# Optimization experiments

Measured on AMD Instinct MI355X. Metric: run time of the kernel, lower is better.

The kernel has to match this reference:

```python
import jax, jax.numpy as jnp
import numpy as np

NUM_EMBEDDINGS = 1024
EMBEDDING_DIM = 256
COMMITMENT_COST = 0.25
DECAY = 0.99
EPSILON = 1e-05


def setup_inputs() -> dict:
    key = jax.random.key(0)
    k1, k2, k3 = jax.random.split(key, 3)
    z = jax.random.normal(k1, (32, EMBEDDING_DIM, 32, 32), dtype=jnp.float32)
    codebook = jax.random.normal(k2, (NUM_EMBEDDINGS, EMBEDDING_DIM), dtype=jnp.float32)
    ema_cluster_size = jnp.zeros((NUM_EMBEDDINGS,), dtype=jnp.float32)
    ema_dw = jax.random.normal(k3, (NUM_EMBEDDINGS, EMBEDDING_DIM), dtype=jnp.float32)
    return {"z": z, "codebook": codebook, "ema_cluster_size": ema_cluster_size, "ema_dw": ema_dw}


def reference(z, codebook, ema_cluster_size, ema_dw):
    K, D = codebook.shape
    # (B,C,H,W) -> (B,H,W,C)
    zp = jnp.transpose(z, (0, 2, 3, 1))
    z_flat = zp.reshape(-1, D)  # [N, D]
    N = z_flat.shape[0]

    # squared L2 distances to each code: [N, K]
    distances = (jnp.sum(z_flat ** 2, axis=1, keepdims=True)
                 + jnp.sum(codebook ** 2, axis=1)
                 - 2.0 * z_flat @ codebook.T)
    idx = jnp.argmin(distances, axis=1)  # [N]

    quantized = codebook[idx].reshape(zp.shape)  # [B,H,W,C]

    # training-mode EMA codebook update (one-hot scatter expressed as segment sums)
    counts = jax.ops.segment_sum(jnp.ones((N,), z_flat.dtype), idx, num_segments=K)  # encodings.sum(0)
    dw = jax.ops.segment_sum(z_flat, idx, num_segments=K)                            # encodings.T @ z_flat
    new_cluster_size = ema_cluster_size * DECAY + (1.0 - DECAY) * counts
    new_ema_dw = ema_dw * DECAY + (1.0 - DECAY) * dw
    n = jnp.sum(new_cluster_size)
    cluster_size = (new_cluster_size + EPSILON) / (n + K * EPSILON) * n
    new_codebook = new_ema_dw / cluster_size[:, None]

    commitment_loss = jnp.mean((zp - jax.lax.stop_gradient(quantized)) ** 2)
    loss = COMMITMENT_COST * commitment_loss

    # straight-through estimator
    quantized_st = zp + jax.lax.stop_gradient(quantized - zp)

    avg_probs = counts / N
    perplexity = jnp.exp(-jnp.sum(avg_probs * jnp.log(avg_probs + 1e-10)))

    quantized_out = jnp.transpose(quantized_st, (0, 3, 1, 2))  # back to (B,C,H,W)
    return (quantized_out, loss, perplexity, new_codebook, new_cluster_size, new_ema_dw)
```

## Files before the change

### kernel.cpp

```cpp
#include <hip/hip_runtime.h>
#include <cfloat>
#include <cstdint>

#define B_BATCH 32
#define D_DIM   256
#define HW      1024
#define N_POS   32768
#define K_CODES 1024
#define DECAY_F   0.99f
#define ONE_M_DECAY 0.01f
#define EPS_F   1e-5f

#define OUT_Q    0
#define OUT_LOSS 8388608
#define OUT_PERP 8388609
#define OUT_CB   8388610
#define OUT_NCS  8650754
#define OUT_EDW  8651778


#define WS_COUNTS  0
#define WS_ZNORM   4096
#define WS_BSUM    4100
#define WS_MEMSET  4104
#define WS_CBNORM  4352
#define WS_OFFS    8448
#define WS_CURSOR  12544
#define WS_IDX     16640
#define WS_SORTED  147712
#define WS_CBHI    278784
#define WS_CBLO    803072
#define WS_PART    1327360
#define WS_SCODE   3424512
#define WS_TOTAL   3555584

typedef short s16x8 __attribute__((ext_vector_type(8)));
typedef float f32x4 __attribute__((ext_vector_type(4)));
typedef unsigned long long u64;

__device__ __forceinline__ ushort f2bf_rne(float x) {
    uint u = __float_as_uint(x);
    uint r = (u + 0x7FFF + ((u >> 16) & 1)) >> 16;
    return (ushort)r;
}
__device__ __forceinline__ float bf2f(ushort h) {
    return __uint_as_float(((uint)h) << 16);
}

__device__ __forceinline__ void gload16(const void* g, void* l) {
    __builtin_amdgcn_global_load_lds(
        (const __attribute__((address_space(1))) unsigned*)(uintptr_t)g,
        (__attribute__((address_space(3))) unsigned*)(uintptr_t)l, 16, 0, 0);
}

__global__ __launch_bounds__(256) void prep_ztrans(const float* __restrict__ z,
                                                   const float* __restrict__ cb,
                                                   ushort* __restrict__ zhi,
                                                   ushort* __restrict__ zlo,
                                                   ushort* __restrict__ cbhi,
                                                   ushort* __restrict__ cblo,
                                                   float* __restrict__ cbnorm,
                                                   float* __restrict__ znorm_acc) {
    __shared__ float Zs[32][68];
    __shared__ float red[256];
    const int tid = threadIdx.x;

    if (blockIdx.x >= 512) {
        int wave = tid >> 6;
        int lane = tid & 63;
        int k = (blockIdx.x - 512) * 4 + wave;
        float4 v = *(const float4*)&cb[(size_t)k * D_DIM + lane * 4];
        ushort4 h, l;
        h.x = f2bf_rne(v.x); l.x = f2bf_rne(v.x - bf2f(h.x));
        h.y = f2bf_rne(v.y); l.y = f2bf_rne(v.y - bf2f(h.y));
        h.z = f2bf_rne(v.z); l.z = f2bf_rne(v.z - bf2f(h.z));
        h.w = f2bf_rne(v.w); l.w = f2bf_rne(v.w - bf2f(h.w));
        *(ushort4*)&cbhi[(size_t)k * D_DIM + lane * 4] = h;
        *(ushort4*)&cblo[(size_t)k * D_DIM + lane * 4] = l;
        float s = v.x * v.x + v.y * v.y + v.z * v.z + v.w * v.w;
        #pragma unroll
        for (int off = 32; off >= 1; off >>= 1) s += __shfl_xor(s, off);
        if (lane == 0) cbnorm[k] = s;
        return;
    }

    const int n0  = blockIdx.x * 64;
    const int b   = n0 >> 10;
    const int hw0 = n0 & 1023;
    const float* zb = z + (size_t)b * (D_DIM * HW) + hw0;

    const int zd  = tid >> 4;
    const int zcg = tid & 15;
    const int n   = tid >> 2;
    const int dq  = tid & 3;
    const int zcol = (((n >> 2) ^ (dq << 1)) << 2) | (n & 3);
    float zsum = 0.f;

    for (int d0 = 0; d0 < D_DIM; d0 += 32) {
        __syncthreads();
        #pragma unroll
        for (int p = 0; p < 2; ++p) {
            int d = zd + p * 16;
            int g = zcg ^ (((d >> 3) & 3) << 1);
            float4 v = *(const float4*)&zb[(size_t)(d0 + d) * HW + zcg * 4];
            *(float4*)&Zs[d][g * 4] = v;
        }
        __syncthreads();
        s16x8 hv, lv;
        #pragma unroll
        for (int j = 0; j < 8; ++j) {
            float f = Zs[dq * 8 + j][zcol];
            zsum += f * f;
            ushort hb = f2bf_rne(f);
            ushort lb = f2bf_rne(f - bf2f(hb));
            hv[j] = (short)hb;
            lv[j] = (short)lb;
        }
        *(s16x8*)&zhi[(size_t)(n0 + n) * D_DIM + d0 + dq * 8] = hv;
        *(s16x8*)&zlo[(size_t)(n0 + n) * D_DIM + d0 + dq * 8] = lv;
    }
    red[tid] = zsum;
    __syncthreads();
    for (int s2 = 128; s2 >= 1; s2 >>= 1) {
        if (tid < s2) red[tid] += red[tid + s2];
        __syncthreads();
    }
    if (tid == 0) atomicAdd(znorm_acc, red[0]);
}

__global__ __launch_bounds__(512, 2) void argmin_gemm(const ushort* __restrict__ cbhi,
                                                      const ushort* __restrict__ cblo,
                                                      const ushort* __restrict__ zhi,
                                                      const ushort* __restrict__ zlo,
                                                      const float* __restrict__ cbnorm,
                                                      u64* __restrict__ partial) {
    __shared__ __align__(16) ushort lds[65536];

    const int tid  = threadIdx.x;
    const int wave = tid >> 6;
    const int lane = tid & 63;
    const int col  = lane & 15;
    const int lg   = lane >> 4;
    const int wr   = wave >> 2;
    const int wc   = wave & 3;
    const int blk  = blockIdx.x;
    const int mt = (blk >> 3) & 3;
    const int pt = (blk & 7) | ((blk >> 5) << 3);

    const int srow = tid >> 2;
    const int G    = tid & 3;
    const int sg   = (G ^ ((srow >> 1) & 3)) * 16;
    const char* pAh = (const char*)cbhi + (size_t)(mt * 256 + srow) * 512 + sg;
    const char* pAl = (const char*)cblo + (size_t)(mt * 256 + srow) * 512 + sg;
    const char* pBh = (const char*)zhi  + (size_t)(pt * 256 + srow) * 512 + sg;
    const char* pBl = (const char*)zlo  + (size_t)(pt * 256 + srow) * 512 + sg;
    char* const ldsw = (char*)lds + wave * 1024;

    auto stage_q = [&](int kt, int bsel, int q) {
        char* d = ldsw + bsel * 65536;
        const int kb = kt * 64;
        if (q == 0)      { gload16(pAh + kb, d);         gload16(pAh + kb + 65536, d + 8192);  }
        else if (q == 1) { gload16(pAl + kb, d + 16384); gload16(pAl + kb + 65536, d + 24576); }
        else if (q == 2) { gload16(pBh + kb, d + 32768); gload16(pBh + kb + 65536, d + 40960); }
        else             { gload16(pBl + kb, d + 49152); gload16(pBl + kb + 65536, d + 57344); }
    };

    const char* ldsc = (const char*)lds;
    const int swz  = (lg ^ ((col >> 1) & 3)) * 16;
    const int aoff = (wr * 128 + col) * 64 + swz;
    const int boff = (wc * 64 + col) * 64 + swz;

    f32x4 acc[8][4];
    #pragma unroll
    for (int mi = 0; mi < 8; ++mi)
        #pragma unroll
        for (int ni = 0; ni < 4; ++ni) acc[mi][ni] = {0.f, 0.f, 0.f, 0.f};

    stage_q(0, 0, 0); stage_q(0, 0, 1); stage_q(0, 0, 2); stage_q(0, 0, 3);

#define MM3A(AH, AL, mi, ni)                                                                   \
    acc[mi][ni] = __builtin_amdgcn_mfma_f32_16x16x32_bf16(AH, bh[ni], acc[mi][ni], 0, 0, 0);   \
    acc[mi][ni] = __builtin_amdgcn_mfma_f32_16x16x32_bf16(AH, bl[ni], acc[mi][ni], 0, 0, 0);   \
    acc[mi][ni] = __builtin_amdgcn_mfma_f32_16x16x32_bf16(AL, bh[ni], acc[mi][ni], 0, 0, 0);
#define ROW3(AH, AL, mi) MM3A(AH, AL, mi, 0) MM3A(AH, AL, mi, 1) MM3A(AH, AL, mi, 2) MM3A(AH, AL, mi, 3)

    #pragma unroll
    for (int t = 0; t < 8; ++t) {
        asm volatile("s_waitcnt vmcnt(0)" ::: "memory");
        __builtin_amdgcn_s_barrier();
        __builtin_amdgcn_sched_barrier(0);

        const char* bp = ldsc + (t & 1) * 65536;
        const int nb = (t + 1) & 1;
        s16x8 bh[4], bl[4];
        s16x8 ah0, al0, ah1, al1;

        bh[0] = *(const s16x8*)(bp + 32768 + boff);
        bl[0] = *(const s16x8*)(bp + 49152 + boff);
        bh[1] = *(const s16x8*)(bp + 32768 + boff + 1024);
        bl[1] = *(const s16x8*)(bp + 49152 + boff + 1024);
        bh[2] = *(const s16x8*)(bp + 32768 + boff + 2048);
        bl[2] = *(const s16x8*)(bp + 49152 + boff + 2048);
        bh[3] = *(const s16x8*)(bp + 32768 + boff + 3072);
        bl[3] = *(const s16x8*)(bp + 49152 + boff + 3072);
        ah0 = *(const s16x8*)(bp + aoff);
        al0 = *(const s16x8*)(bp + 16384 + aoff);
        ah1 = *(const s16x8*)(bp + aoff + 1024);
        al1 = *(const s16x8*)(bp + 16384 + aoff + 1024);
        if (t < 7) stage_q(t + 1, nb, 0);
        __builtin_amdgcn_s_setprio(1);
        ROW3(ah0, al0, 0) ROW3(ah1, al1, 1)
        __builtin_amdgcn_s_setprio(0);

        ah0 = *(const s16x8*)(bp + aoff + 2048);
        al0 = *(const s16x8*)(bp + 16384 + aoff + 2048);
        ah1 = *(const s16x8*)(bp + aoff + 3072);
        al1 = *(const s16x8*)(bp + 16384 + aoff + 3072);
        if (t < 7) stage_q(t + 1, nb, 1);
        __builtin_amdgcn_s_setprio(1);
        ROW3(ah0, al0, 2) ROW3(ah1, al1, 3)
        __builtin_amdgcn_s_setprio(0);

        ah0 = *(const s16x8*)(bp + aoff + 4096);
        al0 = *(const s16x8*)(bp + 16384 + aoff + 4096);
        ah1 = *(const s16x8*)(bp + aoff + 5120);
        al1 = *(const s16x8*)(bp + 16384 + aoff + 5120);
        if (t < 7) stage_q(t + 1, nb, 2);
        __builtin_amdgcn_s_setprio(1);
        ROW3(ah0, al0, 4) ROW3(ah1, al1, 5)
        __builtin_amdgcn_s_setprio(0);

        ah0 = *(const s16x8*)(bp + aoff + 6144);
        al0 = *(const s16x8*)(bp + 16384 + aoff + 6144);
        ah1 = *(const s16x8*)(bp + aoff + 7168);
        al1 = *(const s16x8*)(bp + 16384 + aoff + 7168);
        if (t < 7) stage_q(t + 1, nb, 3);
        __builtin_amdgcn_s_setprio(1);
        ROW3(ah0, al0, 6) ROW3(ah1, al1, 7)
        __builtin_amdgcn_s_setprio(0);
    }
#undef ROW3
#undef MM3A

    const int kbase = mt * 256 + wr * 128;
    u64 best[4] = {~0ull, ~0ull, ~0ull, ~0ull};
    #pragma unroll
    for (int mi = 0; mi < 8; ++mi) {
        float4 cn = *(const float4*)&cbnorm[kbase + mi * 16 + lg * 4];
        const float* cnp = (const float*)&cn;
        #pragma unroll
        for (int ni = 0; ni < 4; ++ni) {
            #pragma unroll
            for (int r = 0; r < 4; ++r) {
                float dist = cnp[r] - 2.f * acc[mi][ni][r];
                uint ub = __float_as_uint(dist);
                ub = ub ^ (uint)(((int)ub >> 31) | 0x80000000);
                u64 key = ((u64)ub << 32) | (uint)(kbase + mi * 16 + lg * 4 + r);
                if (key < best[ni]) best[ni] = key;
            }
        }
    }
    #pragma unroll
    for (int ni = 0; ni < 4; ++ni) {
        u64 o = __shfl_xor(best[ni], 16); if (o < best[ni]) best[ni] = o;
        o = __shfl_xor(best[ni], 32); if (o < best[ni]) best[ni] = o;
    }
    u64* kredp = (u64*)lds;
    if (lane < 16) {
        #pragma unroll
        for (int ni = 0; ni < 4; ++ni)
            kredp[(wc * 64 + ni * 16 + lane) * 2 + wr] = best[ni];
    }
    __syncthreads();
    if (tid < 256) {
        u64 a = kredp[tid * 2 + 0];
        u64 b = kredp[tid * 2 + 1]; if (b < a) a = b;
        partial[(size_t)(pt * 256 + tid) * 4 + mt] = a;
    }
}

__global__ __launch_bounds__(256) void combine_kernel(const u64* __restrict__ partial,
                                                      int* __restrict__ idx,
                                                      float* __restrict__ counts,
                                                      float* __restrict__ bsum_acc) {
    __shared__ int hist[1024];
    __shared__ float red[256];
    const int tid = threadIdx.x;
    for (int j = tid; j < 1024; j += 256) hist[j] = 0;
    __syncthreads();
    int n = blockIdx.x * 256 + tid;
    const u64* p = partial + (size_t)n * 4;
    u64 m = p[0];
    #pragma unroll
    for (int j = 1; j < 4; ++j) { u64 v = p[j]; if (v < m) m = v; }
    int k = (int)(m & 1023u);
    idx[n] = k;
    atomicAdd(&hist[k], 1);
    uint ub = (uint)(m >> 32);
    uint u = (ub & 0x80000000u) ? (ub ^ 0x80000000u) : ~ub;
    red[tid] = __uint_as_float(u);
    __syncthreads();
    for (int s2 = 128; s2 >= 1; s2 >>= 1) {
        if (tid < s2) red[tid] += red[tid + s2];
        __syncthreads();
    }
    if (tid == 0) atomicAdd(bsum_acc, red[0]);
    for (int j = tid; j < 1024; j += 256) {
        int c = hist[j];
        if (c) atomicAdd(&counts[j], (float)c);
    }
}

__global__ __launch_bounds__(1024) void small_kernel(const float* __restrict__ ema_cs,
                                                     const float* __restrict__ counts,
                                                     const float* __restrict__ znorm,
                                                     const float* __restrict__ bsum,
                                                     float* __restrict__ out_ncs,
                                                     float* __restrict__ out_perp,
                                                     float* __restrict__ out_loss,
                                                     float* __restrict__ ntot_ws,
                                                     int* __restrict__ offsets,
                                                     int* __restrict__ cursor) {
    __shared__ float s1[1024];
    __shared__ float s2[1024];
    __shared__ int   s3[1024];
    int k = threadIdx.x;
    float cnt = counts[k];
    float ncs = ema_cs[k] * DECAY_F + ONE_M_DECAY * cnt;
    out_ncs[k] = ncs;
    float p = cnt / (float)N_POS;
    s1[k] = ncs;
    s2[k] = p * logf(p + 1e-10f);
    int c = (int)cnt;
    s3[k] = c;
    __syncthreads();
    for (int off = 1; off < 1024; off <<= 1) {
        int v = (k >= off) ? s3[k - off] : 0;
        __syncthreads();
        s3[k] += v;
        __syncthreads();
    }
    int excl = s3[k] - c;
    offsets[k] = excl;
    cursor[k] = excl;
    for (int st = 512; st >= 1; st >>= 1) {
        if (k < st) { s1[k] += s1[k + st]; s2[k] += s2[k + st]; }
        __syncthreads();
    }
    if (k == 0) {
        ntot_ws[0] = s1[0];
        out_perp[0] = expf(-s2[0]);
        out_loss[0] = 0.25f * (znorm[0] + bsum[0]) / 8388608.0f;
    }
}

__global__ __launch_bounds__(256) void scatter_kernel(const int* __restrict__ idx,
                                                      int* __restrict__ cursor,
                                                      int* __restrict__ sorted,
                                                      int* __restrict__ scode,
                                                      float* __restrict__ dw_zero) {
    __shared__ int hist[1024];
    __shared__ int base_s[1024];
    const int tid = threadIdx.x;
    {
        float4 z4 = {0.f, 0.f, 0.f, 0.f};
        size_t e = ((size_t)blockIdx.x * 256 + tid) * 8;
        *(float4*)&dw_zero[e] = z4;
        *(float4*)&dw_zero[e + 4] = z4;
    }
    for (int j = tid; j < 1024; j += 256) hist[j] = 0;
    __syncthreads();
    int n = blockIdx.x * 256 + tid;
    int k = idx[n];
    atomicAdd(&hist[k], 1);
    __syncthreads();
    for (int j = tid; j < 1024; j += 256) {
        int c = hist[j];
        if (c) base_s[j] = atomicAdd(&cursor[j], c);
        hist[j] = 0;
    }
    __syncthreads();
    int rank = atomicAdd(&hist[k], 1);
    int pos = base_s[k] + rank;
    sorted[pos] = n;
    scode[pos] = k;
}

#define DW_CHUNK 64
__global__ __launch_bounds__(256) void dw_chunk_kernel(const ushort* __restrict__ zhi,
                                                       const ushort* __restrict__ zlo,
                                                       const int* __restrict__ sorted,
                                                       const int* __restrict__ scode,
                                                       const int* __restrict__ offsets,
                                                       const float* __restrict__ counts,
                                                       float* __restrict__ dw) {
    __shared__ int sid[DW_CHUNK];
    __shared__ int sk[DW_CHUNK];
    const int tid = threadIdx.x;
    const int p0 = blockIdx.x * DW_CHUNK;
    if (tid < DW_CHUNK) {
        sid[tid] = sorted[p0 + tid];
        sk[tid]  = scode[p0 + tid];
    }
    __syncthreads();
    float acc = 0.f;
    int runstart = 0;
    #pragma unroll 4
    for (int i = 0; i < DW_CHUNK; ++i) {
        int id = sid[i];
        float zv = bf2f(zhi[(size_t)id * D_DIM + tid]) + bf2f(zlo[(size_t)id * D_DIM + tid]);
        acc += zv;
        bool end = (i == DW_CHUNK - 1) || (sk[i + 1] != sk[i]);
        if (end) {
            int k = sk[i];
            int off = offsets[k];
            int cnt = (int)counts[k];
            if (p0 + runstart == off && p0 + i == off + cnt - 1)
                dw[(size_t)k * D_DIM + tid] = acc;
            else
                atomicAdd(&dw[(size_t)k * D_DIM + tid], acc);
            acc = 0.f;
            runstart = i + 1;
        }
    }
}

__global__ __launch_bounds__(256) void tail_fused(const float* __restrict__ cb,
                                                  const int* __restrict__ idx,
                                                  float* __restrict__ outq,
                                                  const float* __restrict__ ema_dw,
                                                  const float* __restrict__ out_ncs,
                                                  const float* __restrict__ ntot_ws,
                                                  float* __restrict__ out_edw,
                                                  float* __restrict__ out_cb) {
    const int tid = threadIdx.x;
    if (blockIdx.x >= 512) {
        int k = blockIdx.x - 512;
        int d = tid;
        float ncs = out_ncs[k];
        float nt = ntot_ws[0];
        float csz = (ncs + EPS_F) / (nt + (float)K_CODES * EPS_F) * nt;
        size_t e = (size_t)k * D_DIM + d;
        float ed = ema_dw[e] * DECAY_F + ONE_M_DECAY * out_edw[e];
        out_edw[e] = ed;
        out_cb[e] = ed / csz;
        return;
    }

    __shared__ float Qs[32][65];
    __shared__ int kidx[64];
    const int n0  = blockIdx.x * 64;
    const int b   = n0 >> 10;
    const int hw0 = n0 & 1023;
    float* ob = outq + (size_t)b * (D_DIM * HW) + hw0;

    if (tid < 64) kidx[tid] = idx[n0 + tid];

    for (int d0 = 0; d0 < D_DIM; d0 += 32) {
        __syncthreads();
        #pragma unroll
        for (int h = 0; h < 2; ++h) {
            int s  = tid + 256 * h;
            int n  = s >> 3;
            int dq = s & 7;
            int k  = kidx[n];
            float4 q = *(const float4*)&cb[(size_t)k * D_DIM + d0 + dq * 4];
            Qs[dq * 4 + 0][n] = q.x;
            Qs[dq * 4 + 1][n] = q.y;
            Qs[dq * 4 + 2][n] = q.z;
            Qs[dq * 4 + 3][n] = q.w;
        }
        __syncthreads();
        #pragma unroll
        for (int j = 0; j < 8; ++j) {
            int v = tid + 256 * j;
            int d = v >> 6;
            int n = v & 63;
            ob[(size_t)(d0 + d) * HW + n] = Qs[d][n];
        }
    }
}

extern "C" void kernel_launch(void* const* d_in, const int* in_sizes, int n_in,
                              void* d_out, int out_size, void* d_ws, size_t ws_size,
                              hipStream_t stream) {
    const float* z       = (const float*)d_in[0];
    const float* cb      = (const float*)d_in[1];
    const float* ema_cs  = (const float*)d_in[2];
    const float* ema_dw  = (const float*)d_in[3];
    float* out = (float*)d_out;

    char* ws = (char*)d_ws;
    float* ws_counts = (float*)(ws + WS_COUNTS);
    float* ws_znorm  = (float*)(ws + WS_ZNORM);
    float* ws_bsum   = (float*)(ws + WS_BSUM);
    float* ws_cbnorm = (float*)(ws + WS_CBNORM);
    int*   ws_offs   = (int*)(ws + WS_OFFS);
    int*   ws_cursor = (int*)(ws + WS_CURSOR);
    int*   ws_idx    = (int*)(ws + WS_IDX);
    int*   ws_sorted = (int*)(ws + WS_SORTED);
    ushort* ws_cbhi  = (ushort*)(ws + WS_CBHI);
    ushort* ws_cblo  = (ushort*)(ws + WS_CBLO);
    u64*   ws_part   = (u64*)(ws + WS_PART);
    int*   ws_scode  = (int*)(ws + WS_SCODE);

    ushort* zhi = (ushort*)out;
    ushort* zlo = zhi + 8388608;

    hipMemsetAsync(d_ws, 0, WS_MEMSET, stream);

    prep_ztrans<<<768, 256, 0, stream>>>(z, cb, zhi, zlo, ws_cbhi, ws_cblo,
                                         ws_cbnorm, ws_znorm);
    argmin_gemm<<<512, 512, 0, stream>>>(ws_cbhi, ws_cblo, zhi, zlo, ws_cbnorm, ws_part);
    combine_kernel<<<N_POS / 256, 256, 0, stream>>>(ws_part, ws_idx, ws_counts, ws_bsum);
    small_kernel<<<1, 1024, 0, stream>>>(ema_cs, ws_counts, ws_znorm, ws_bsum,
                                         out + OUT_NCS, out + OUT_PERP, out + OUT_LOSS,
                                         (float*)(ws + WS_ZNORM) + 1024, ws_offs, ws_cursor);
    scatter_kernel<<<N_POS / 256, 256, 0, stream>>>(ws_idx, ws_cursor, ws_sorted,
                                                    ws_scode, out + OUT_EDW);
    dw_chunk_kernel<<<N_POS / DW_CHUNK, 256, 0, stream>>>(zhi, zlo, ws_sorted, ws_scode,
                                                          ws_offs, ws_counts, out + OUT_EDW);
    tail_fused<<<1536, 256, 0, stream>>>(cb, ws_idx, out + OUT_Q, ema_dw, out + OUT_NCS,
                                         (float*)(ws + WS_ZNORM) + 1024,
                                         out + OUT_EDW, out + OUT_CB);
}
```

Before: 196.8 us.

## Shrink argmin GEMM tile to 256x128 with triple-buffered LDS prefetch

The argmin GEMM block changes from 512 threads with a 256x256 tile to 256 threads with a 256-code by 128-position tile, doubling the grid to 1024 blocks. Staging moves from quartered loads into a double buffer to a three-stage LDS ring that prefetches two k-steps ahead and waits with a partial vmcnt instead of draining all loads. The aim is to hide global load latency better and raise block count. In exchange each codebook tile is reloaded twice as often relative to z, and one block per CU with a larger LDS footprint may lower occupancy.

```diff
diff --git a/kernel.cpp b/kernel.cpp
--- a/kernel.cpp
+++ b/kernel.cpp
@@ -128,21 +128,21 @@
     if (tid == 0) atomicAdd(znorm_acc, red[0]);
 }
 
-__global__ __launch_bounds__(512, 2) void argmin_gemm(const ushort* __restrict__ cbhi,
+__global__ __launch_bounds__(256, 1) void argmin_gemm(const ushort* __restrict__ cbhi,
                                                       const ushort* __restrict__ cblo,
                                                       const ushort* __restrict__ zhi,
                                                       const ushort* __restrict__ zlo,
                                                       const float* __restrict__ cbnorm,
                                                       u64* __restrict__ partial) {
-    __shared__ __align__(16) ushort lds[65536];
+    __shared__ __align__(16) ushort lds[73728];
 
     const int tid  = threadIdx.x;
     const int wave = tid >> 6;
     const int lane = tid & 63;
     const int col  = lane & 15;
     const int lg   = lane >> 4;
-    const int wr   = wave >> 2;
-    const int wc   = wave & 3;
+    const int wr   = wave >> 1;
+    const int wc   = wave & 1;
     const int blk  = blockIdx.x;
     const int mt = (blk >> 3) & 3;
     const int pt = (blk & 7) | ((blk >> 5) << 3);
@@ -152,17 +152,25 @@
     const int sg   = (G ^ ((srow >> 1) & 3)) * 16;
     const char* pAh = (const char*)cbhi + (size_t)(mt * 256 + srow) * 512 + sg;
     const char* pAl = (const char*)cblo + (size_t)(mt * 256 + srow) * 512 + sg;
-    const char* pBh = (const char*)zhi  + (size_t)(pt * 256 + srow) * 512 + sg;
-    const char* pBl = (const char*)zlo  + (size_t)(pt * 256 + srow) * 512 + sg;
+    const char* pBh = (const char*)zhi  + (size_t)(pt * 128 + srow) * 512 + sg;
+    const char* pBl = (const char*)zlo  + (size_t)(pt * 128 + srow) * 512 + sg;
     char* const ldsw = (char*)lds + wave * 1024;
 
-    auto stage_q = [&](int kt, int bsel, int q) {
-        char* d = ldsw + bsel * 65536;
+    auto stage_all = [&](int kt, int bsel) {
+        char* d = ldsw + bsel * 49152;
         const int kb = kt * 64;
-        if (q == 0)      { gload16(pAh + kb, d);         gload16(pAh + kb + 65536, d + 8192);  }
-        else if (q == 1) { gload16(pAl + kb, d + 16384); gload16(pAl + kb + 65536, d + 24576); }
-        else if (q == 2) { gload16(pBh + kb, d + 32768); gload16(pBh + kb + 65536, d + 40960); }
-        else             { gload16(pBl + kb, d + 49152); gload16(pBl + kb + 65536, d + 57344); }
+        gload16(pAh + kb,         d);
+        gload16(pAh + kb + 32768, d + 4096);
+        gload16(pAh + kb + 65536, d + 8192);
+        gload16(pAh + kb + 98304, d + 12288);
+        gload16(pAl + kb,         d + 16384);
+        gload16(pAl + kb + 32768, d + 20480);
+        gload16(pAl + kb + 65536, d + 24576);
+        gload16(pAl + kb + 98304, d + 28672);
+        gload16(pBh + kb,         d + 32768);
+        gload16(pBh + kb + 32768, d + 36864);
+        gload16(pBl + kb,         d + 40960);
+        gload16(pBl + kb + 32768, d + 45056);
     };
 
     const char* ldsc = (const char*)lds;
@@ -176,7 +184,8 @@
         #pragma unroll
         for (int ni = 0; ni < 4; ++ni) acc[mi][ni] = {0.f, 0.f, 0.f, 0.f};
 
-    stage_q(0, 0, 0); stage_q(0, 0, 1); stage_q(0, 0, 2); stage_q(0, 0, 3);
+    stage_all(0, 0);
+    stage_all(1, 1);
 
 #define MM3A(AH, AL, mi, ni)                                                                   \
     acc[mi][ni] = __builtin_amdgcn_mfma_f32_16x16x32_bf16(AH, bh[ni], acc[mi][ni], 0, 0, 0);   \
@@ -186,28 +195,29 @@
 
     #pragma unroll
     for (int t = 0; t < 8; ++t) {
-        asm volatile("s_waitcnt vmcnt(0)" ::: "memory");
+        if (t < 7) asm volatile("s_waitcnt vmcnt(12)" ::: "memory");
+        else       asm volatile("s_waitcnt vmcnt(0)" ::: "memory");
         __builtin_amdgcn_s_barrier();
         __builtin_amdgcn_sched_barrier(0);
 
-        const char* bp = ldsc + (t & 1) * 65536;
-        const int nb = (t + 1) & 1;
+        if (t < 6) stage_all(t + 2, (t + 2) % 3);
+
+        const char* bp = ldsc + (t % 3) * 49152;
         s16x8 bh[4], bl[4];
         s16x8 ah0, al0, ah1, al1;
 
         bh[0] = *(const s16x8*)(bp + 32768 + boff);
-        bl[0] = *(const s16x8*)(bp + 49152 + boff);
+        bl[0] = *(const s16x8*)(bp + 40960 + boff);
         bh[1] = *(const s16x8*)(bp + 32768 + boff + 1024);
-        bl[1] = *(const s16x8*)(bp + 49152 + boff + 1024);
+        bl[1] = *(const s16x8*)(bp + 40960 + boff + 1024);
         bh[2] = *(const s16x8*)(bp + 32768 + boff + 2048);
-        bl[2] = *(const s16x8*)(bp + 49152 + boff + 2048);
+        bl[2] = *(const s16x8*)(bp + 40960 + boff + 2048);
         bh[3] = *(const s16x8*)(bp + 32768 + boff + 3072);
-        bl[3] = *(const s16x8*)(bp + 49152 + boff + 3072);
+        bl[3] = *(const s16x8*)(bp + 40960 + boff + 3072);
         ah0 = *(const s16x8*)(bp + aoff);
         al0 = *(const s16x8*)(bp + 16384 + aoff);
         ah1 = *(const s16x8*)(bp + aoff + 1024);
         al1 = *(const s16x8*)(bp + 16384 + aoff + 1024);
-        if (t < 7) stage_q(t + 1, nb, 0);
         __builtin_amdgcn_s_setprio(1);
         ROW3(ah0, al0, 0) ROW3(ah1, al1, 1)
         __builtin_amdgcn_s_setprio(0);
@@ -216,7 +226,6 @@
         al0 = *(const s16x8*)(bp + 16384 + aoff + 2048);
         ah1 = *(const s16x8*)(bp + aoff + 3072);
         al1 = *(const s16x8*)(bp + 16384 + aoff + 3072);
-        if (t < 7) stage_q(t + 1, nb, 1);
         __builtin_amdgcn_s_setprio(1);
         ROW3(ah0, al0, 2) ROW3(ah1, al1, 3)
         __builtin_amdgcn_s_setprio(0);
@@ -225,7 +234,6 @@
         al0 = *(const s16x8*)(bp + 16384 + aoff + 4096);
         ah1 = *(const s16x8*)(bp + aoff + 5120);
         al1 = *(const s16x8*)(bp + 16384 + aoff + 5120);
-        if (t < 7) stage_q(t + 1, nb, 2);
         __builtin_amdgcn_s_setprio(1);
         ROW3(ah0, al0, 4) ROW3(ah1, al1, 5)
         __builtin_amdgcn_s_setprio(0);
@@ -234,7 +242,6 @@
         al0 = *(const s16x8*)(bp + 16384 + aoff + 6144);
         ah1 = *(const s16x8*)(bp + aoff + 7168);
         al1 = *(const s16x8*)(bp + 16384 + aoff + 7168);
-        if (t < 7) stage_q(t + 1, nb, 3);
         __builtin_amdgcn_s_setprio(1);
         ROW3(ah0, al0, 6) ROW3(ah1, al1, 7)
         __builtin_amdgcn_s_setprio(0);
@@ -272,10 +279,10 @@
             kredp[(wc * 64 + ni * 16 + lane) * 2 + wr] = best[ni];
     }
     __syncthreads();
-    if (tid < 256) {
+    if (tid < 128) {
         u64 a = kredp[tid * 2 + 0];
         u64 b = kredp[tid * 2 + 1]; if (b < a) a = b;
-        partial[(size_t)(pt * 256 + tid) * 4 + mt] = a;
+        partial[(size_t)(pt * 128 + tid) * 4 + mt] = a;
     }
 }
 
@@ -511,7 +518,7 @@
 
     prep_ztrans<<<768, 256, 0, stream>>>(z, cb, zhi, zlo, ws_cbhi, ws_cblo,
                                          ws_cbnorm, ws_znorm);
-    argmin_gemm<<<512, 512, 0, stream>>>(ws_cbhi, ws_cblo, zhi, zlo, ws_cbnorm, ws_part);
+    argmin_gemm<<<1024, 256, 0, stream>>>(ws_cbhi, ws_cblo, zhi, zlo, ws_cbnorm, ws_part);
     combine_kernel<<<N_POS / 256, 256, 0, stream>>>(ws_part, ws_idx, ws_counts, ws_bsum);
     small_kernel<<<1, 1024, 0, stream>>>(ema_cs, ws_counts, ws_znorm, ws_bsum,
                                          out + OUT_NCS, out + OUT_PERP, out + OUT_LOSS,
```

Result: slower. 209.6 us (+6.5%).
